# Kernel tuning notes

Measured on AMD Instinct MI355X. Metric: run time of the kernel, lower is better.

The kernel has to match this reference:

```python
import jax, jax.numpy as jnp
import numpy as np

T_STEPS = 4
TAU = 2.0
EPS = 1e-5
NUM_HEADS = 8
SCALE = 0.125  # hardcoded self.scale in the torch module
SG_ALPHA = 4.0  # spikingjelly default sigmoid surrogate alpha


@jax.custom_vjp
def heaviside(x):
    return (x >= 0.0).astype(x.dtype)

def _hv_fwd(x):
    return heaviside(x), x

def _hv_bwd(x, g):
    s = jax.nn.sigmoid(SG_ALPHA * x)
    return (g * SG_ALPHA * s * (1.0 - s),)

heaviside.defvjp(_hv_fwd, _hv_bwd)


def lif(x_seq, v_th):
    # MultiStepLIFNode: v += (x - v)/tau; spike = H(v - v_th); hard reset to 0 (detached).
    def step(v, x):
        v = v + (x - v) / TAU
        s = heaviside(v - v_th)
        v = v * (1.0 - jax.lax.stop_gradient(s))
        return v, s
    _, out = jax.lax.scan(step, jnp.zeros_like(x_seq[0]), x_seq)
    return out


def bn(x, g, b):
    # BatchNorm1d training-mode stats over (batch, length) per channel; x: (TB, C, N)
    m = jnp.mean(x, axis=(0, 2), keepdims=True)
    var = jnp.mean((x - m) ** 2, axis=(0, 2), keepdims=True)
    return g[None, :, None] * (x - m) * jax.lax.rsqrt(var + EPS) + b[None, :, None]


def _branch(x, w, b, g, beta):
    # linear over channel dim + BN + LIF, then split heads -> (T,B,H,N,d)
    T, B, C, N = x.shape
    y = jnp.einsum('oc,tbcn->tbon', w, x) + b[None, None, :, None]
    y = bn(y.reshape(T * B, C, N), g, beta).reshape(T, B, C, N)
    y = lif(y, 1.0)
    d = C // NUM_HEADS
    return y.transpose(0, 1, 3, 2).reshape(T, B, N, NUM_HEADS, d).transpose(0, 1, 3, 2, 4)


def setup_inputs() -> dict:
    key = jax.random.key(0)
    ks = jax.random.split(key, 6)
    B, C, N = 8, 512, 1024
    bound = float(np.sqrt(6.0 / (3 * C + C)))  # xavier_uniform for (3C, C)
    return {
        'q': jax.random.normal(ks[0], (B, C, N), jnp.float32),
        'k': jax.random.normal(ks[1], (B, C, N), jnp.float32),
        'v': jax.random.normal(ks[2], (B, C, N), jnp.float32),
        'in_proj_w': jax.random.uniform(ks[3], (3 * C, C), jnp.float32, -bound, bound),
        'in_proj_b': jnp.zeros((3 * C,), jnp.float32),
        'q_gamma': jnp.ones((C,), jnp.float32),
        'q_beta': jnp.zeros((C,), jnp.float32),
        'k_gamma': jnp.ones((C,), jnp.float32),
        'k_beta': jnp.zeros((C,), jnp.float32),
        'v_gamma': jnp.ones((C,), jnp.float32),
        'v_beta': jnp.zeros((C,), jnp.float32),
        'proj_w': jax.random.normal(ks[4], (C, C), jnp.float32) * (1.0 / np.sqrt(C)),
        'proj_b': jnp.zeros((C,), jnp.float32),
        'p_gamma': jnp.ones((C,), jnp.float32),
        'p_beta': jnp.zeros((C,), jnp.float32),
    }


def reference(q, k, v, in_proj_w, in_proj_b, q_gamma, q_beta, k_gamma, k_beta,
              v_gamma, v_beta, proj_w, proj_b, p_gamma, p_beta):
    B, C, N = q.shape
    qs = jnp.broadcast_to(q[None], (T_STEPS, B, C, N))
    ks_ = jnp.broadcast_to(k[None], (T_STEPS, B, C, N))
    vs = jnp.broadcast_to(v[None], (T_STEPS, B, C, N))

    qh = _branch(qs, in_proj_w[:C], in_proj_b[:C], q_gamma, q_beta)        # (T,B,H,N,d)
    kh = _branch(ks_, in_proj_w[C:2 * C], in_proj_b[C:2 * C], k_gamma, k_beta)
    vh = _branch(vs, in_proj_w[2 * C:], in_proj_b[2 * C:], v_gamma, v_beta)

    # linear attention: (k^T v) then q @ (k^T v)
    ktv = jnp.einsum('tbhnd,tbhne->tbhde', kh, vh)            # (T,B,H,d,d)
    att = jnp.einsum('tbhnd,tbhde->tbhne', qh, ktv) * SCALE   # (T,B,H,N,d)

    x = att.transpose(0, 1, 2, 4, 3).reshape(T_STEPS, B, C, N)
    x = lif(x, 0.5)  # attn_lif with v_threshold=0.5

    z = jnp.einsum('oc,tbcn->tbon', proj_w, x) + proj_b[None, None, :, None]  # 1x1 conv
    z = bn(z.reshape(T_STEPS * B, C, N), p_gamma, p_beta).reshape(T_STEPS, B, C, N)
    return lif(z, 1.0)
```

## Files before the change

### kernel.cpp

```cpp
#include <hip/hip_runtime.h>

#define C    512
#define NDIM 1024
#define BDIM 8
#define TDIM 4
#define HDIM 8
#define CN   (C*NDIM)
#define BCN  (BDIM*CN)

typedef unsigned short u16;
typedef unsigned int   u32;
typedef unsigned long long u64;
typedef __attribute__((ext_vector_type(8))) short bf8v;
typedef __attribute__((ext_vector_type(4))) float f4v;

__device__ __forceinline__ u16 f2bf(float f) {
    u32 u = __float_as_uint(f);
    u32 r = u + 0x7FFFu + ((u >> 16) & 1u);
    return (u16)(r >> 16);
}
__device__ __forceinline__ float bf2f(u16 h) { return __uint_as_float((u32)h << 16); }

#if defined(__has_builtin)
#if __has_builtin(__builtin_amdgcn_global_load_lds)
#define HAS_GLL 1
#endif
#endif
#ifdef HAS_GLL
#define GLD(gp, lp) __builtin_amdgcn_global_load_lds( \
    (const __attribute__((address_space(1))) u32*)(gp), \
    (__attribute__((address_space(3))) u32*)(lp), 16, 0, 0)
#else
#define GLD(gp, lp) (*(uint4*)(lp) = *(const uint4*)(const void*)(gp))
#endif

__global__ __launch_bounds__(256) void gemm_in_k(
    const float* __restrict__ W, const float* __restrict__ bias,
    const float* __restrict__ X, float* __restrict__ Y, int rowOff)
{
    __shared__ float As[16][68];
    __shared__ float Bs[16][68];
    const int tid = threadIdx.x;
    const int b  = blockIdx.z;
    const int m0 = blockIdx.y * 64;
    const int n0 = blockIdx.x * 64;
    const float* Xb = X + (size_t)b * CN;

    const int am = tid >> 2;
    const int ak = (tid & 3) * 4;
    const int bk = tid >> 4;
    const int bn = (tid & 15) * 4;
    const int tx = tid & 15, ty = tid >> 4;

    float acc[4][4];
    #pragma unroll
    for (int i = 0; i < 4; i++)
        #pragma unroll
        for (int j = 0; j < 4; j++) acc[i][j] = 0.f;

    for (int k0 = 0; k0 < C; k0 += 16) {
        float4 a  = *(const float4*)&W [(size_t)(rowOff + m0 + am) * C + k0 + ak];
        float4 bb = *(const float4*)&Xb[(size_t)(k0 + bk) * NDIM + n0 + bn];
        __syncthreads();
        As[ak + 0][am] = a.x; As[ak + 1][am] = a.y;
        As[ak + 2][am] = a.z; As[ak + 3][am] = a.w;
        *(float4*)&Bs[bk][bn] = bb;
        __syncthreads();
        #pragma unroll
        for (int k = 0; k < 16; k++) {
            float av[4], bv[4];
            *(float4*)av = *(const float4*)&As[k][ty * 4];
            *(float4*)bv = *(const float4*)&Bs[k][tx * 4];
            #pragma unroll
            for (int i = 0; i < 4; i++)
                #pragma unroll
                for (int j = 0; j < 4; j++)
                    acc[i][j] += av[i] * bv[j];
        }
    }
    #pragma unroll
    for (int i = 0; i < 4; i++) {
        float bsv = bias[rowOff + m0 + ty * 4 + i];
        float4 o4 = make_float4(acc[i][0] + bsv, acc[i][1] + bsv,
                                acc[i][2] + bsv, acc[i][3] + bsv);
        *(float4*)&Y[(size_t)b * CN + (size_t)(m0 + ty * 4 + i) * NDIM + n0 + tx * 4] = o4;
    }
}

__global__ __launch_bounds__(256) void split_pw_k(
    const float* __restrict__ PW, u16* __restrict__ Ps)
{
    const int idx = blockIdx.x * 256 + threadIdx.x;
    float x = PW[idx];
    u16 h1 = f2bf(x); float r1 = x - bf2f(h1);
    u16 h2 = f2bf(r1); float r2 = r1 - bf2f(h2);
    u16 h3 = f2bf(r2);
    Ps[idx] = h1; Ps[idx + 262144] = h2; Ps[idx + 2 * 262144] = h3;
}

__global__ __launch_bounds__(256, 2) void gemm_proj_mfma(
    const u16* __restrict__ Ps, const unsigned char* __restrict__ spkT,
    float* __restrict__ Z)
{
    __shared__ __align__(16) u16 Ab[2][12288];
    __shared__ __align__(16) u16 Bb[2][4096];
    const int tid = threadIdx.x;
    const int zb = blockIdx.z, t = zb >> 3, bb = zb & 7;
    const int m0 = blockIdx.y * 128, n0 = blockIdx.x * 128;

    u32 aoff[2][3];
    int lofs[2];
    #pragma unroll
    for (int r = 0; r < 2; r++) {
        const int cid = tid + (r << 8);
        const int mm = cid & 15, kg = (cid >> 4) & 3, mt = cid >> 6;
        lofs[r] = cid * 8;
        #pragma unroll
        for (int s = 0; s < 3; s++)
            aoff[r][s] = (u32)s * 262144u + (u32)(m0 + mt * 16 + mm) * 512u + kg * 8;
    }
    auto stageA = [&](int ki2, int p2) {
        const u32 kk = (u32)ki2 << 5;
        #pragma unroll
        for (int r = 0; r < 2; r++)
            #pragma unroll
            for (int s = 0; s < 3; s++)
                GLD(Ps + aoff[r][s] + kk, &Ab[p2][s * 4096 + lofs[r]]);
    };
    const int nn = tid & 15, ntl = (tid >> 4) & 7, seg = tid >> 7;
    const u32 srcB = ((u32)bb * 1024u + (u32)(n0 + ntl * 16 + nn)) * 512u + seg * 16;
    const int ldsB0 = (ntl * 64 + seg * 32 + nn) * 8;
    auto convB = [&](uint4 braw, int p2) {
        u32 bs[4] = {braw.x, braw.y, braw.z, braw.w};
        u32 w[8];
        #pragma unroll
        for (int qq = 0; qq < 4; qq++) {
            u32 v = bs[qq] >> t;
            w[qq * 2 + 0] = ((v & 1u) ? 0x3F80u : 0u) | ((v & 0x100u) ? 0x3F800000u : 0u);
            w[qq * 2 + 1] = (((v >> 16) & 1u) ? 0x3F80u : 0u) | ((v & 0x1000000u) ? 0x3F800000u : 0u);
        }
        *(uint4*)&Bb[p2][ldsB0]       = make_uint4(w[0], w[1], w[2], w[3]);
        *(uint4*)&Bb[p2][ldsB0 + 128] = make_uint4(w[4], w[5], w[6], w[7]);
    };

    const int lane = tid & 63, wv = tid >> 6;
    const int wm = wv >> 1, wn = wv & 1;
    const int q = lane >> 4, ln = lane & 15;
    int afo[4], bfo[4];
    #pragma unroll
    for (int i = 0; i < 4; i++) {
        afo[i] = ((wm * 4 + i) * 64 + q * 16 + ln) * 8;
        bfo[i] = ((wn * 4 + i) * 64 + q * 16 + ln) * 8;
    }

    f4v acc[4][4];
    #pragma unroll
    for (int i = 0; i < 4; i++)
        #pragma unroll
        for (int j = 0; j < 4; j++) acc[i][j] = (f4v){0.f, 0.f, 0.f, 0.f};

    stageA(0, 0);
    convB(*(const uint4*)&spkT[srcB], 0);
    uint4 braw;
    for (int ki = 0; ki < 16; ki++) {
        const int p = ki & 1;
        __syncthreads();
        if (ki < 15) {
            stageA(ki + 1, p ^ 1);
            braw = *(const uint4*)&spkT[srcB + ((u32)(ki + 1) << 5)];
        }
        bf8v bf[4];
        #pragma unroll
        for (int j = 0; j < 4; j++) bf[j] = *(const bf8v*)&Bb[p][bfo[j]];
        #pragma unroll
        for (int sa = 0; sa < 3; sa++) {
            bf8v af[4];
            #pragma unroll
            for (int i = 0; i < 4; i++) af[i] = *(const bf8v*)&Ab[p][sa * 4096 + afo[i]];
            #pragma unroll
            for (int i = 0; i < 4; i++)
                #pragma unroll
                for (int j = 0; j < 4; j++)
                    acc[i][j] = __builtin_amdgcn_mfma_f32_16x16x32_bf16(af[i], bf[j], acc[i][j], 0, 0, 0);
        }
        if (ki < 15) convB(braw, p ^ 1);
    }
    float* Zb = Z + (size_t)zb * CN;
    #pragma unroll
    for (int i = 0; i < 4; i++) {
        const int row = m0 + (wm * 4 + i) * 16 + q * 4;
        #pragma unroll
        for (int g = 0; g < 4; g++) {
            float* zr = Zb + (size_t)(row + g) * 1024 + n0 + ln;
            #pragma unroll
            for (int j = 0; j < 4; j++)
                zr[(wn * 4 + j) * 16] = acc[i][j][g];
        }
    }
}

__global__ __launch_bounds__(256) void chan_sum_k(
    const float* __restrict__ X, float* __restrict__ mean, int outer)
{
    __shared__ float red[256];
    const int o = blockIdx.x, tid = threadIdx.x;
    const int total = outer * NDIM;
    float s = 0.f;
    for (int i = tid; i < total; i += 256) {
        int ou = i >> 10, n = i & 1023;
        s += X[(size_t)(ou * C + o) * NDIM + n];
    }
    red[tid] = s; __syncthreads();
    for (int off = 128; off > 0; off >>= 1) {
        if (tid < off) red[tid] += red[tid + off];
        __syncthreads();
    }
    if (tid == 0) mean[o] = red[0] / (float)total;
}

__global__ __launch_bounds__(256) void chan_var_k(
    const float* __restrict__ X, const float* __restrict__ mean,
    float* __restrict__ rstd, int outer)
{
    __shared__ float red[256];
    const int o = blockIdx.x, tid = threadIdx.x;
    const int total = outer * NDIM;
    const float m = mean[o];
    float s = 0.f;
    for (int i = tid; i < total; i += 256) {
        int ou = i >> 10, n = i & 1023;
        float d = X[(size_t)(ou * C + o) * NDIM + n] - m;
        s += d * d;
    }
    red[tid] = s; __syncthreads();
    for (int off = 128; off > 0; off >>= 1) {
        if (tid < off) red[tid] += red[tid + off];
        __syncthreads();
    }
    if (tid == 0) rstd[o] = 1.f / sqrtf(red[0] / (float)total + 1e-5f);
}

__global__ __launch_bounds__(256) void bn_lif_pack_k(
    const float* __restrict__ Y, const float* __restrict__ mean,
    const float* __restrict__ rstd, const float* __restrict__ gamma,
    const float* __restrict__ beta, unsigned char* __restrict__ spk)
{
    const int idx = blockIdx.x * 256 + threadIdx.x;
    const int o = (idx >> 10) & (C - 1);
    float y = Y[idx];
    float x = gamma[o] * (y - mean[o]);
    x = x * rstd[o] + beta[o];
    float v = 0.f; unsigned bits = 0;
    #pragma unroll
    for (int t = 0; t < 4; t++) {
        v += (x - v) * 0.5f;
        if (v - 1.0f >= 0.f) { bits |= (1u << t); v = 0.f; }
    }
    spk[idx] = (unsigned char)bits;
}

__global__ __launch_bounds__(256) void qpack_k(
    const unsigned char* __restrict__ spk, u64* __restrict__ qm)
{
    __shared__ unsigned char tile[64][80];
    const int tid = threadIdx.x;
    const int bh = blockIdx.x; const int h = bh & 7, b = bh >> 3;
    const int n0 = blockIdx.y * 64;
    {
        int dd = tid >> 2, sg = tid & 3;
        *(uint4*)&tile[dd][sg * 16] =
            *(const uint4*)&spk[(size_t)(b * C + h * 64 + dd) * NDIM + n0 + sg * 16];
    }
    __syncthreads();
    const int lane = tid & 63, wv = tid >> 6;
    for (int i = 0; i < 16; i++) {
        int j = wv * 16 + i;
        unsigned s = tile[lane][j];
        #pragma unroll
        for (int t = 0; t < 4; t++) {
            u64 m = __ballot((s >> t) & 1);
            if (lane == t)
                qm[(size_t)((t * BDIM + b) * HDIM + h) * NDIM + n0 + j] = m;
        }
    }
}

__global__ __launch_bounds__(256) void kv_pack_k(
    const unsigned char* __restrict__ spk, u64* __restrict__ bits)
{
    const int tid = threadIdx.x;
    const int gw = blockIdx.x * 4 + (tid >> 6);
    const int lane = tid & 63;
    const int w = gw & 15, c = (gw >> 4) & (C - 1), b = gw >> 13;
    unsigned s = spk[(size_t)(b * C + c) * NDIM + w * 64 + lane];
    #pragma unroll
    for (int t = 0; t < 4; t++) {
        u64 m = __ballot((s >> t) & 1);
        if (lane == t)
            bits[(size_t)((t * BDIM + b) * C + c) * 16 + w] = m;
    }
}

__global__ __launch_bounds__(256) void ktv_k(
    const u64* __restrict__ kb, const u64* __restrict__ vb,
    u16* __restrict__ ktv)
{
    __shared__ u64 ks[64][17];
    __shared__ u64 vs[64][17];
    const int tid = threadIdx.x;
    const int g = blockIdx.x;
    const int h = g & 7, b = (g >> 3) & 7, t = g >> 6;
    const size_t base = ((size_t)(t * BDIM + b) * C + h * 64) * 16;
    {
        int r = tid >> 2, w0 = (tid & 3) * 4;
        #pragma unroll
        for (int j = 0; j < 4; j++) {
            ks[r][w0 + j] = kb[base + r * 16 + w0 + j];
            vs[r][w0 + j] = vb[base + r * 16 + w0 + j];
        }
    }
    __syncthreads();
    const int dd = tid >> 2, e0 = (tid & 3) * 16;
    u64 kr[16];
    #pragma unroll
    for (int w = 0; w < 16; w++) kr[w] = ks[dd][w];
    #pragma unroll
    for (int i = 0; i < 16; i++) {
        int e = e0 + i;
        int s = 0;
        #pragma unroll
        for (int w = 0; w < 16; w++) s += __popcll(kr[w] & vs[e][w]);
        ktv[(size_t)(g * 64 + dd) * 64 + e] = (u16)s;
    }
}

__global__ __launch_bounds__(256) void att_lif_k(
    const u16* __restrict__ ktv, const u64* __restrict__ qm,
    unsigned char* __restrict__ spkT)
{
    __shared__ u16 ks[4][64][64];
    const int tid = threadIdx.x;
    const int bh = blockIdx.x; const int h = bh & 7, b = bh >> 3;
    const int n0 = blockIdx.y * 64;
    #pragma unroll
    for (int t = 0; t < 4; t++) {
        const u32* src = (const u32*)&ktv[(size_t)((t * BDIM + b) * HDIM + h) * 4096];
        u32* dst = (u32*)&ks[t][0][0];
        #pragma unroll
        for (int j = 0; j < 8; j++) dst[tid + 256 * j] = src[tid + 256 * j];
    }
    __syncthreads();
    const int lane = tid & 63, wv = tid >> 6;
    for (int i = 0; i < 16; i++) {
        const int n = n0 + wv * 16 + i;
        float v = 0.f; unsigned bits = 0;
        #pragma unroll
        for (int t = 0; t < 4; t++) {
            u64 m = qm[(size_t)((t * BDIM + b) * HDIM + h) * NDIM + n];
            int acc = 0;
            while (m) {
                int dd = __ffsll(m) - 1;
                m &= m - 1;
                acc += ks[t][dd][lane];
            }
            float x = (float)acc * 0.125f;
            v += (x - v) * 0.5f;
            if (v - 0.5f >= 0.f) { bits |= (1u << t); v = 0.f; }
        }
        spkT[((size_t)b * 1024 + n) * 512 + h * 64 + lane] = (unsigned char)bits;
    }
}

__global__ __launch_bounds__(256) void final_bn_lif_k(
    float* __restrict__ Z, const float* __restrict__ mean,
    const float* __restrict__ rstd, const float* __restrict__ gamma,
    const float* __restrict__ beta)
{
    const int idx = blockIdx.x * 256 + threadIdx.x;
    const int o = (idx >> 10) & (C - 1);
    const float m = mean[o], rs = rstd[o], g = gamma[o], bt = beta[o];
    float v = 0.f;
    float outs[4];
    #pragma unroll
    for (int t = 0; t < 4; t++) {
        float z = Z[(size_t)t * BCN + idx];
        float x = g * (z - m);
        x = x * rs + bt;
        v += (x - v) * 0.5f;
        float s = (v - 1.0f >= 0.f) ? 1.f : 0.f;
        v *= (1.f - s);
        outs[t] = s;
    }
    #pragma unroll
    for (int t = 0; t < 4; t++) Z[(size_t)t * BCN + idx] = outs[t];
}

extern "C" void kernel_launch(void* const* d_in, const int* in_sizes, int n_in,
                              void* d_out, int out_size, void* d_ws, size_t ws_size,
                              hipStream_t stream)
{
    const float* q     = (const float*)d_in[0];
    const float* k     = (const float*)d_in[1];
    const float* v     = (const float*)d_in[2];
    const float* W     = (const float*)d_in[3];
    const float* Wb    = (const float*)d_in[4];
    const float* qg    = (const float*)d_in[5];
    const float* qb    = (const float*)d_in[6];
    const float* kg    = (const float*)d_in[7];
    const float* kbt   = (const float*)d_in[8];
    const float* vg    = (const float*)d_in[9];
    const float* vbt   = (const float*)d_in[10];
    const float* pw    = (const float*)d_in[11];
    const float* pg    = (const float*)d_in[13];
    const float* pbeta = (const float*)d_in[14];

    char* p = (char*)d_ws;
    float* Y = (float*)p;                   p += (size_t)BCN * 4;
    unsigned char* spk = (unsigned char*)p; p += (size_t)BCN;
    u64* qmv = (u64*)p;                     p += (size_t)TDIM * BDIM * HDIM * NDIM * 8;
    u64* kbits = (u64*)p;                   p += (size_t)TDIM * BDIM * C * 16 * 8;
    u64* vbits = (u64*)p;                   p += (size_t)TDIM * BDIM * C * 16 * 8;
    u16* ktv = (u16*)p;                     p += (size_t)TDIM * BDIM * HDIM * 64 * 64 * 2;
    float* mean = (float*)p;                p += 4096;
    float* rstd = (float*)p;                p += 4096;

    u16* Ps = (u16*)qmv;
    unsigned char* spkT = spk;
    float* outF = (float*)d_out;

    const float* Xs[3] = {q, k, v};
    const float* Gs[3] = {qg, kg, vg};
    const float* Bt[3] = {qb, kbt, vbt};

    for (int br = 0; br < 3; ++br) {
        gemm_in_k<<<dim3(16, 8, 8), 256, 0, stream>>>(W, Wb, Xs[br], Y, br * C);
        chan_sum_k<<<C, 256, 0, stream>>>(Y, mean, BDIM);
        chan_var_k<<<C, 256, 0, stream>>>(Y, mean, rstd, BDIM);
        bn_lif_pack_k<<<BCN / 256, 256, 0, stream>>>(Y, mean, rstd, Gs[br], Bt[br], spk);
        if (br == 0)
            qpack_k<<<dim3(64, 16), 256, 0, stream>>>(spk, qmv);
        else
            kv_pack_k<<<16384, 256, 0, stream>>>(spk, br == 1 ? kbits : vbits);
    }
    ktv_k<<<256, 256, 0, stream>>>(kbits, vbits, ktv);
    att_lif_k<<<dim3(64, 16), 256, 0, stream>>>(ktv, qmv, spkT);
    split_pw_k<<<1024, 256, 0, stream>>>(pw, Ps);
    gemm_proj_mfma<<<dim3(8, 4, 32), 256, 0, stream>>>(Ps, spkT, outF);
    chan_sum_k<<<C, 256, 0, stream>>>(outF, mean, TDIM * BDIM);
    chan_var_k<<<C, 256, 0, stream>>>(outF, mean, rstd, TDIM * BDIM);
    final_bn_lif_k<<<BCN / 256, 256, 0, stream>>>(outF, mean, rstd, pg, pbeta);
}
```

Measured before the change: 645.3 us.

## Batch q/k/v input projections and BN stats into single launches

```diff
diff --git a/kernel.cpp b/kernel.cpp
--- a/kernel.cpp
+++ b/kernel.cpp
@@ -34,56 +34,66 @@
 #define GLD(gp, lp) (*(uint4*)(lp) = *(const uint4*)(const void*)(gp))
 #endif
 
-__global__ __launch_bounds__(256) void gemm_in_k(
+__global__ __launch_bounds__(256) void gemm_in3_k(
     const float* __restrict__ W, const float* __restrict__ bias,
-    const float* __restrict__ X, float* __restrict__ Y, int rowOff)
+    const float* __restrict__ Xq, const float* __restrict__ Xk,
+    const float* __restrict__ Xv, float* __restrict__ Y3)
 {
     __shared__ float As[16][68];
-    __shared__ float Bs[16][68];
-    const int tid = threadIdx.x;
-    const int b  = blockIdx.z;
+    __shared__ float Bs[16][136];
+    const int tid = threadIdx.x;
+    const int bz = blockIdx.z;
+    const int br = bz >> 3, b = bz & 7;
     const int m0 = blockIdx.y * 64;
-    const int n0 = blockIdx.x * 64;
-    const float* Xb = X + (size_t)b * CN;
+    const int n0 = blockIdx.x * 128;
+    const float* Xb = (br == 0 ? Xq : (br == 1 ? Xk : Xv)) + (size_t)b * CN;
+    const int rowOff = br * 512;
 
     const int am = tid >> 2;
     const int ak = (tid & 3) * 4;
     const int bk = tid >> 4;
-    const int bn = (tid & 15) * 4;
+    const int bn = (tid & 15) * 8;
     const int tx = tid & 15, ty = tid >> 4;
 
-    float acc[4][4];
+    float acc[4][8];
     #pragma unroll
     for (int i = 0; i < 4; i++)
         #pragma unroll
-        for (int j = 0; j < 4; j++) acc[i][j] = 0.f;
-
-    for (int k0 = 0; k0 < C; k0 += 16) {
-        float4 a  = *(const float4*)&W [(size_t)(rowOff + m0 + am) * C + k0 + ak];
-        float4 bb = *(const float4*)&Xb[(size_t)(k0 + bk) * NDIM + n0 + bn];
+        for (int j = 0; j < 8; j++) acc[i][j] = 0.f;
+
+    for (int k0 = 0; k0 < 512; k0 += 16) {
+        float4 a  = *(const float4*)&W [(size_t)(rowOff + m0 + am) * 512 + k0 + ak];
+        float4 b0 = *(const float4*)&Xb[(size_t)(k0 + bk) * NDIM + n0 + bn];
+        float4 b1 = *(const float4*)&Xb[(size_t)(k0 + bk) * NDIM + n0 + bn + 4];
         __syncthreads();
         As[ak + 0][am] = a.x; As[ak + 1][am] = a.y;
         As[ak + 2][am] = a.z; As[ak + 3][am] = a.w;
-        *(float4*)&Bs[bk][bn] = bb;
+        *(float4*)&Bs[bk][bn]     = b0;
+        *(float4*)&Bs[bk][bn + 4] = b1;
         __syncthreads();
         #pragma unroll
         for (int k = 0; k < 16; k++) {
-            float av[4], bv[4];
+            float av[4], bv[8];
             *(float4*)av = *(const float4*)&As[k][ty * 4];
-            *(float4*)bv = *(const float4*)&Bs[k][tx * 4];
+            *(float4*)&bv[0] = *(const float4*)&Bs[k][tx * 8];
+            *(float4*)&bv[4] = *(const float4*)&Bs[k][tx * 8 + 4];
             #pragma unroll
             for (int i = 0; i < 4; i++)
                 #pragma unroll
-                for (int j = 0; j < 4; j++)
+                for (int j = 0; j < 8; j++)
                     acc[i][j] += av[i] * bv[j];
         }
     }
     #pragma unroll
     for (int i = 0; i < 4; i++) {
         float bsv = bias[rowOff + m0 + ty * 4 + i];
-        float4 o4 = make_float4(acc[i][0] + bsv, acc[i][1] + bsv,
+        float* yr = Y3 + (size_t)bz * CN + (size_t)(m0 + ty * 4 + i) * NDIM + n0 + tx * 8;
+        float4 o0 = make_float4(acc[i][0] + bsv, acc[i][1] + bsv,
                                 acc[i][2] + bsv, acc[i][3] + bsv);
-        *(float4*)&Y[(size_t)b * CN + (size_t)(m0 + ty * 4 + i) * NDIM + n0 + tx * 4] = o4;
+        float4 o1 = make_float4(acc[i][4] + bsv, acc[i][5] + bsv,
+                                acc[i][6] + bsv, acc[i][7] + bsv);
+        *(float4*)&yr[0] = o0;
+        *(float4*)&yr[4] = o1;
     }
 }
 
@@ -199,11 +209,14 @@
     }
 }
 
-__global__ __launch_bounds__(256) void chan_sum_k(
-    const float* __restrict__ X, float* __restrict__ mean, int outer)
+__global__ __launch_bounds__(256) void chan_sum3_k(
+    const float* __restrict__ X3, float* __restrict__ mean3, int outer)
 {
     __shared__ float red[256];
-    const int o = blockIdx.x, tid = threadIdx.x;
+    const int gb = blockIdx.x;
+    const int o = gb & (C - 1);
+    const float* X = X3 + (size_t)(gb >> 9) * BCN;
+    const int tid = threadIdx.x;
     const int total = outer * NDIM;
     float s = 0.f;
     for (int i = tid; i < total; i += 256) {
@@ -215,17 +228,20 @@
         if (tid < off) red[tid] += red[tid + off];
         __syncthreads();
     }
-    if (tid == 0) mean[o] = red[0] / (float)total;
-}
-
-__global__ __launch_bounds__(256) void chan_var_k(
-    const float* __restrict__ X, const float* __restrict__ mean,
-    float* __restrict__ rstd, int outer)
+    if (tid == 0) mean3[gb] = red[0] / (float)total;
+}
+
+__global__ __launch_bounds__(256) void chan_var3_k(
+    const float* __restrict__ X3, const float* __restrict__ mean3,
+    float* __restrict__ rstd3, int outer)
 {
     __shared__ float red[256];
-    const int o = blockIdx.x, tid = threadIdx.x;
+    const int gb = blockIdx.x;
+    const int o = gb & (C - 1);
+    const float* X = X3 + (size_t)(gb >> 9) * BCN;
+    const int tid = threadIdx.x;
     const int total = outer * NDIM;
-    const float m = mean[o];
+    const float m = mean3[gb];
     float s = 0.f;
     for (int i = tid; i < total; i += 256) {
         int ou = i >> 10, n = i & 1023;
@@ -237,7 +253,7 @@
         if (tid < off) red[tid] += red[tid + off];
         __syncthreads();
     }
-    if (tid == 0) rstd[o] = 1.f / sqrtf(red[0] / (float)total + 1e-5f);
+    if (tid == 0) rstd3[gb] = 1.f / sqrtf(red[0] / (float)total + 1e-5f);
 }
 
 __global__ __launch_bounds__(256) void bn_lif_pack_k(
@@ -415,28 +431,28 @@
     const float* pbeta = (const float*)d_in[14];
 
     char* p = (char*)d_ws;
-    float* Y = (float*)p;                   p += (size_t)BCN * 4;
     unsigned char* spk = (unsigned char*)p; p += (size_t)BCN;
     u64* qmv = (u64*)p;                     p += (size_t)TDIM * BDIM * HDIM * NDIM * 8;
     u64* kbits = (u64*)p;                   p += (size_t)TDIM * BDIM * C * 16 * 8;
     u64* vbits = (u64*)p;                   p += (size_t)TDIM * BDIM * C * 16 * 8;
     u16* ktv = (u16*)p;                     p += (size_t)TDIM * BDIM * HDIM * 64 * 64 * 2;
-    float* mean = (float*)p;                p += 4096;
-    float* rstd = (float*)p;                p += 4096;
-
+    float* mean3 = (float*)p;               p += 8192;
+    float* rstd3 = (float*)p;               p += 8192;
+
+    float* Y3 = (float*)d_out;
+    float* outF = (float*)d_out;
     u16* Ps = (u16*)qmv;
     unsigned char* spkT = spk;
-    float* outF = (float*)d_out;
-
-    const float* Xs[3] = {q, k, v};
+
     const float* Gs[3] = {qg, kg, vg};
     const float* Bt[3] = {qb, kbt, vbt};
 
+    gemm_in3_k<<<dim3(8, 8, 24), 256, 0, stream>>>(W, Wb, q, k, v, Y3);
+    chan_sum3_k<<<3 * C, 256, 0, stream>>>(Y3, mean3, BDIM);
+    chan_var3_k<<<3 * C, 256, 0, stream>>>(Y3, mean3, rstd3, BDIM);
     for (int br = 0; br < 3; ++br) {
-        gemm_in_k<<<dim3(16, 8, 8), 256, 0, stream>>>(W, Wb, Xs[br], Y, br * C);
-        chan_sum_k<<<C, 256, 0, stream>>>(Y, mean, BDIM);
-        chan_var_k<<<C, 256, 0, stream>>>(Y, mean, rstd, BDIM);
-        bn_lif_pack_k<<<BCN / 256, 256, 0, stream>>>(Y, mean, rstd, Gs[br], Bt[br], spk);
+        bn_lif_pack_k<<<BCN / 256, 256, 0, stream>>>(Y3 + (size_t)br * BCN,
+            mean3 + br * C, rstd3 + br * C, Gs[br], Bt[br], spk);
         if (br == 0)
             qpack_k<<<dim3(64, 16), 256, 0, stream>>>(spk, qmv);
         else
@@ -446,7 +462,7 @@
     att_lif_k<<<dim3(64, 16), 256, 0, stream>>>(ktv, qmv, spkT);
     split_pw_k<<<1024, 256, 0, stream>>>(pw, Ps);
     gemm_proj_mfma<<<dim3(8, 4, 32), 256, 0, stream>>>(Ps, spkT, outF);
-    chan_sum_k<<<C, 256, 0, stream>>>(outF, mean, TDIM * BDIM);
-    chan_var_k<<<C, 256, 0, stream>>>(outF, mean, rstd, TDIM * BDIM);
-    final_bn_lif_k<<<BCN / 256, 256, 0, stream>>>(outF, mean, rstd, pg, pbeta);
-}
+    chan_sum3_k<<<C, 256, 0, stream>>>(outF, mean3, TDIM * BDIM);
+    chan_var3_k<<<C, 256, 0, stream>>>(outF, mean3, rstd3, TDIM * BDIM);
+    final_bn_lif_k<<<BCN / 256, 256, 0, stream>>>(outF, mean3, rstd3, pg, pbeta);
+}
```

Result: faster. 585.2 us (-9.3%).
